# Kernel optimization log

Hardware: AMD Instinct MI355X
Metric: run time of the kernel (lower is better)

The kernel has to match this reference:

```python
import jax, jax.numpy as jnp
import numpy as np

EPS = 1e-6

def _rmsnorm(x, w):
    var = jnp.mean(x * x, axis=-1, keepdims=True)
    return x * jax.lax.rsqrt(var + EPS) * w

def _act_quant(x):
    # per-token int8 absmax quantization (BitNet b1.58)
    scale = 127.0 / jnp.clip(jnp.max(jnp.abs(x), axis=-1, keepdims=True), 1e-5)
    return jnp.round(jnp.clip(x * scale, -128.0, 127.0)) / scale

def _weight_quant(w):
    # per-tensor ternary quantization with mean-abs scale
    scale = 1.0 / jnp.clip(jnp.mean(jnp.abs(w)), 1e-5)
    return jnp.round(jnp.clip(w * scale, -1.0, 1.0)) / scale

def _ste(x, qfn):
    return x + jax.lax.stop_gradient(qfn(x) - x)

def _bitlinear(x, w):
    xq = _ste(x, _act_quant)
    wq = _ste(w, _weight_quant)
    return jnp.einsum('bsh,fh->bsf', xq, wq)

def setup_inputs() -> dict:
    key = jax.random.key(0)
    k1, k2, k3 = jax.random.split(key, 3)
    B, S, H, F = 4, 4096, 1024, 4096
    x = jax.random.normal(k1, (B, S, H), dtype=jnp.float32)
    norm_w = jnp.ones((H,), dtype=jnp.float32)
    w_up = jax.random.normal(k2, (F, H), dtype=jnp.float32) * (H ** -0.5)
    w_down = jax.random.normal(k3, (H, F), dtype=jnp.float32) * (F ** -0.5)
    return {"x": x, "norm_w": norm_w, "w_up": w_up, "w_down": w_down}

def reference(x, norm_w, w_up, w_down):
    residual = x
    h = _rmsnorm(x, norm_w)
    h = _bitlinear(h, w_up)          # [B,S,F]
    h = jnp.square(jax.nn.relu(h))   # relu^2
    h = _bitlinear(h, w_down)        # [B,S,H]
    return h + residual
```

## Files before the change

kernel.cpp:

```cpp
#include <hip/hip_runtime.h>
#include <hip/hip_fp16.h>

#define M_TOK 16384
#define H_DIM 1024
#define F_DIM 4096

typedef __attribute__((ext_vector_type(4))) int int4v;

static const size_t OFF_H2    = 0;
static const size_t OFF_Q2    = OFF_H2   + 134217728ULL;
static const size_t OFF_XQ    = OFF_Q2   + 67108864ULL;
static const size_t OFF_WQU   = OFF_XQ   + 16777216ULL;
static const size_t OFF_WQD   = OFF_WQU  + 4194304ULL;
static const size_t OFF_DQX   = OFF_WQD  + 4194304ULL;
static const size_t OFF_S2    = OFF_DQX  + 65536ULL;
static const size_t OFF_DQ2   = OFF_S2   + 65536ULL;
static const size_t OFF_PMAX  = OFF_DQ2  + 65536ULL;
static const size_t OFF_WPART = OFF_PMAX + 4194304ULL;
static const size_t OFF_WSC   = OFF_WPART+ 8192ULL;
static const size_t WS_NEEDED = OFF_WSC  + 16ULL;

__device__ __forceinline__ void ldg_lds16(const void* g, void* l) {
  __builtin_amdgcn_global_load_lds(
      (const __attribute__((address_space(1))) void*)g,
      (__attribute__((address_space(3))) void*)l, 16, 0, 0);
}

__global__ __launch_bounds__(256) void k_wabs(const float* __restrict__ wu,
                                              const float* __restrict__ wd,
                                              float* __restrict__ part) {
  const int b = blockIdx.x;
  const float* w = (b < 1024) ? wu : wd;
  const int cb = b & 1023;
  const size_t base = (size_t)cb * 4096 + threadIdx.x * 4;
  float s = 0.0f;
#pragma unroll
  for (int it = 0; it < 4; ++it) {
    const float4 v = *(const float4*)(w + base + it * 1024);
    s += fabsf(v.x) + fabsf(v.y) + fabsf(v.z) + fabsf(v.w);
  }
#pragma unroll
  for (int sh = 32; sh; sh >>= 1) s += __shfl_xor(s, sh, 64);
  __shared__ float red[4];
  if ((threadIdx.x & 63) == 0) red[threadIdx.x >> 6] = s;
  __syncthreads();
  if (threadIdx.x == 0) part[b] = red[0] + red[1] + red[2] + red[3];
}

__global__ __launch_bounds__(256) void k_wscale(const float* __restrict__ part,
                                                float* __restrict__ wsc) {
  const int b = blockIdx.x;
  const float* p = part + b * 1024;
  float s = p[threadIdx.x] + p[threadIdx.x + 256] + p[threadIdx.x + 512] + p[threadIdx.x + 768];
#pragma unroll
  for (int sh = 32; sh; sh >>= 1) s += __shfl_xor(s, sh, 64);
  __shared__ float red[4];
  if ((threadIdx.x & 63) == 0) red[threadIdx.x >> 6] = s;
  __syncthreads();
  if (threadIdx.x == 0) {
    const float mean = (red[0] + red[1] + red[2] + red[3]) * (1.0f / 4194304.0f);
    const float c = fmaxf(mean, 1e-5f);
    wsc[b * 2]     = c;
    wsc[b * 2 + 1] = 1.0f / c;
  }
}

__global__ __launch_bounds__(256) void k_wquant(const float* __restrict__ wu,
                                                const float* __restrict__ wd,
                                                char* __restrict__ qu,
                                                char* __restrict__ qd,
                                                const float* __restrict__ wsc) {
  const size_t t = (size_t)blockIdx.x * 256 + threadIdx.x;
  const float* w; char* q; float scale; size_t i;
  if (t < 1048576) { w = wu; q = qu; scale = wsc[1]; i = t * 4; }
  else             { w = wd; q = qd; scale = wsc[3]; i = (t - 1048576) * 4; }
  const float4 v = *(const float4*)(w + i);
  const int a = (int)rintf(fminf(fmaxf(v.x * scale, -1.0f), 1.0f));
  const int b = (int)rintf(fminf(fmaxf(v.y * scale, -1.0f), 1.0f));
  const int c = (int)rintf(fminf(fmaxf(v.z * scale, -1.0f), 1.0f));
  const int d = (int)rintf(fminf(fmaxf(v.w * scale, -1.0f), 1.0f));
  *(unsigned*)(q + i) = (a & 255) | ((b & 255) << 8) | ((c & 255) << 16) | ((d & 255) << 24);
}

__global__ __launch_bounds__(256) void k_rmsnorm_quant(const float* __restrict__ x,
                                                       const float* __restrict__ nw,
                                                       char* __restrict__ xq,
                                                       float* __restrict__ dqx) {
  const int row = blockIdx.x;
  const int t = threadIdx.x;
  const float4 v = *(const float4*)(x + (size_t)row * H_DIM + t * 4);
  float ss = v.x * v.x + v.y * v.y + v.z * v.z + v.w * v.w;
#pragma unroll
  for (int sh = 32; sh; sh >>= 1) ss += __shfl_xor(ss, sh, 64);
  __shared__ float red[4];
  __shared__ float redm[4];
  if ((t & 63) == 0) red[t >> 6] = ss;
  __syncthreads();
  ss = red[0] + red[1] + red[2] + red[3];
  const float rinv = 1.0f / sqrtf(ss * (1.0f / 1024.0f) + 1e-6f);
  const float4 w4 = *(const float4*)(nw + t * 4);
  float4 n;
  n.x = v.x * rinv * w4.x;  n.y = v.y * rinv * w4.y;
  n.z = v.z * rinv * w4.z;  n.w = v.w * rinv * w4.w;
  float am = fmaxf(fmaxf(fabsf(n.x), fabsf(n.y)), fmaxf(fabsf(n.z), fabsf(n.w)));
#pragma unroll
  for (int sh = 32; sh; sh >>= 1) am = fmaxf(am, __shfl_xor(am, sh, 64));
  if ((t & 63) == 0) redm[t >> 6] = am;
  __syncthreads();
  am = fmaxf(fmaxf(redm[0], redm[1]), fmaxf(redm[2], redm[3]));
  am = fmaxf(am, 1e-5f);
  const float scale = 127.0f / am;
  const int qa = (int)rintf(fminf(fmaxf(n.x * scale, -128.0f), 127.0f));
  const int qb = (int)rintf(fminf(fmaxf(n.y * scale, -128.0f), 127.0f));
  const int qc = (int)rintf(fminf(fmaxf(n.z * scale, -128.0f), 127.0f));
  const int qd = (int)rintf(fminf(fmaxf(n.w * scale, -128.0f), 127.0f));
  *(unsigned*)(xq + (size_t)row * H_DIM + t * 4) =
      (qa & 255) | ((qb & 255) << 8) | ((qc & 255) << 16) | ((qd & 255) << 24);
  if (t == 0) dqx[row] = am * (1.0f / 127.0f);
}

template <int LDA_, int LDB_, int KTILES>
__device__ __forceinline__ void gemm_core(const char* __restrict__ A,
                                          const char* __restrict__ B,
                                          int mBase, int nBase,
                                          char* As, char* Bs, int4v acc[4][4]) {
  const int t = threadIdx.x;
  const int lane = t & 63;
  const int wm = (t >> 6) & 1;
  const int wn = t >> 7;
  const int sRow = t >> 2;
  const int sCol = (t & 3) << 4;
  const char* Ag0 = A + (size_t)(mBase + sRow) * LDA_ + sCol;
  const char* Ag1 = A + (size_t)(mBase + 64 + sRow) * LDA_ + sCol;
  const char* Bg0 = B + (size_t)(nBase + sRow) * LDB_ + sCol;
  const char* Bg1 = B + (size_t)(nBase + 64 + sRow) * LDB_ + sCol;
  char* Al0 = As + t * 16;
  char* Al1 = As + 4096 + t * 16;
  char* Bl0 = Bs + t * 16;
  char* Bl1 = Bs + 4096 + t * 16;
  const int aOff = (wm * 64 + (lane & 15)) * 64 + ((lane >> 4) << 4);
  const int bOff = (wn * 64 + (lane & 15)) * 64 + ((lane >> 4) << 4);

  for (int kt = 0; kt < KTILES; ++kt) {
    __syncthreads();
    ldg_lds16(Ag0, Al0);
    ldg_lds16(Ag1, Al1);
    ldg_lds16(Bg0, Bl0);
    ldg_lds16(Bg1, Bl1);
    Ag0 += 64; Ag1 += 64; Bg0 += 64; Bg1 += 64;
    __syncthreads();
    int4v a[4], b[4];
#pragma unroll
    for (int i = 0; i < 4; ++i) a[i] = *(const int4v*)(As + aOff + i * 16 * 64);
#pragma unroll
    for (int j = 0; j < 4; ++j) b[j] = *(const int4v*)(Bs + bOff + j * 16 * 64);
#pragma unroll
    for (int i = 0; i < 4; ++i)
#pragma unroll
      for (int j = 0; j < 4; ++j)
        acc[i][j] = __builtin_amdgcn_mfma_i32_16x16x64_i8(a[i], b[j], acc[i][j], 0, 0, 0);
  }
}

__global__ __launch_bounds__(256, 2) void k_gemm1(const char* __restrict__ xq,
                                                  const char* __restrict__ wq,
                                                  const float* __restrict__ wsc,
                                                  const float* __restrict__ dqx,
                                                  __half* __restrict__ h2,
                                                  float* __restrict__ pmax) {
  __shared__ char smem[16384];
  int4v acc[4][4];
#pragma unroll
  for (int i = 0; i < 4; ++i)
#pragma unroll
    for (int j = 0; j < 4; ++j) acc[i][j] = (int4v){0, 0, 0, 0};
  const int mBase = blockIdx.y * 128;
  const int nBase = blockIdx.x * 128;
  gemm_core<H_DIM, H_DIM, 16>(xq, wq, mBase, nBase, smem, smem + 8192, acc);

  const int t = threadIdx.x;
  const int lane = t & 63;
  const int wm = (t >> 6) & 1;
  const int wn = t >> 7;
  const float dqw = wsc[0];
#pragma unroll
  for (int i = 0; i < 4; ++i) {
    const int rbase = mBase + wm * 64 + i * 16 + ((lane >> 4) << 2);
    const float4 dq4 = *(const float4*)(dqx + rbase);
    const float* dqp = (const float*)&dq4;
    float rmax[4] = {0.0f, 0.0f, 0.0f, 0.0f};
#pragma unroll
    for (int j = 0; j < 4; ++j) {
      const int col = nBase + wn * 64 + j * 16 + (lane & 15);
#pragma unroll
      for (int r = 0; r < 4; ++r) {
        float v = (float)acc[i][j][r] * dqp[r] * dqw;
        v = fmaxf(v, 0.0f);
        v = v * v;
        const __half h = __float2half(v);
        h2[(size_t)(rbase + r) * F_DIM + col] = h;
        rmax[r] = fmaxf(rmax[r], __half2float(h));
      }
    }
#pragma unroll
    for (int s = 1; s < 16; s <<= 1) {
#pragma unroll
      for (int r = 0; r < 4; ++r) rmax[r] = fmaxf(rmax[r], __shfl_xor(rmax[r], s, 64));
    }
    if ((lane & 15) == 0) {
      const int nb2 = blockIdx.x * 2 + wn;
#pragma unroll
      for (int r = 0; r < 4; ++r) pmax[(size_t)nb2 * M_TOK + rbase + r] = rmax[r];
    }
  }
}

__global__ __launch_bounds__(256) void k_rowred(const float* __restrict__ pmax,
                                                float* __restrict__ scale2,
                                                float* __restrict__ dq2) {
  const int row = blockIdx.x * 256 + threadIdx.x;
  float m = 0.0f;
#pragma unroll
  for (int i = 0; i < 64; ++i) m = fmaxf(m, pmax[(size_t)i * M_TOK + row]);
  m = fmaxf(m, 1e-5f);
  scale2[row] = 127.0f / m;
  dq2[row] = m * (1.0f / 127.0f);
}

__global__ __launch_bounds__(256) void k_quant2(const __half* __restrict__ h2,
                                                const float* __restrict__ scale2,
                                                char* __restrict__ q2) {
  const size_t t = (size_t)blockIdx.x * 256 + threadIdx.x;
  const size_t i = t * 8;
  const int row = (int)(i >> 12);
  const float s = scale2[row];
  __half2 hh[4];
  *(float4*)hh = *(const float4*)(h2 + i);
  int q[8];
#pragma unroll
  for (int k = 0; k < 4; ++k) {
    const float lo = __low2float(hh[k]);
    const float hi = __high2float(hh[k]);
    q[2 * k]     = (int)rintf(fminf(lo * s, 127.0f));
    q[2 * k + 1] = (int)rintf(fminf(hi * s, 127.0f));
  }
  const unsigned u0 = (q[0] & 255) | ((q[1] & 255) << 8) | ((q[2] & 255) << 16) | ((q[3] & 255) << 24);
  const unsigned u1 = (q[4] & 255) | ((q[5] & 255) << 8) | ((q[6] & 255) << 16) | ((q[7] & 255) << 24);
  *(uint2*)(q2 + i) = make_uint2(u0, u1);
}

__global__ __launch_bounds__(256, 2) void k_gemm2(const char* __restrict__ q2,
                                                  const char* __restrict__ wq,
                                                  const float* __restrict__ wsc,
                                                  const float* __restrict__ dq2,
                                                  const float* __restrict__ x,
                                                  float* __restrict__ out) {
  __shared__ char smem[16384];
  int4v acc[4][4];
#pragma unroll
  for (int i = 0; i < 4; ++i)
#pragma unroll
    for (int j = 0; j < 4; ++j) acc[i][j] = (int4v){0, 0, 0, 0};
  const int mBase = blockIdx.y * 128;
  const int nBase = blockIdx.x * 128;
  gemm_core<F_DIM, F_DIM, 64>(q2, wq, mBase, nBase, smem, smem + 8192, acc);

  const int t = threadIdx.x;
  const int lane = t & 63;
  const int wm = (t >> 6) & 1;
  const int wn = t >> 7;
  const float dqw = wsc[2];
#pragma unroll
  for (int i = 0; i < 4; ++i) {
    const int rbase = mBase + wm * 64 + i * 16 + ((lane >> 4) << 2);
    const float4 dq4 = *(const float4*)(dq2 + rbase);
    const float* dqp = (const float*)&dq4;
#pragma unroll
    for (int j = 0; j < 4; ++j) {
      const int col = nBase + wn * 64 + j * 16 + (lane & 15);
#pragma unroll
      for (int r = 0; r < 4; ++r) {
        const size_t idx = (size_t)(rbase + r) * H_DIM + col;
        out[idx] = (float)acc[i][j][r] * dqp[r] * dqw + x[idx];
      }
    }
  }
}

extern "C" void kernel_launch(void* const* d_in, const int* in_sizes, int n_in,
                              void* d_out, int out_size, void* d_ws, size_t ws_size,
                              hipStream_t stream) {
  const float* x  = (const float*)d_in[0];
  const float* nw = (const float*)d_in[1];
  const float* wu = (const float*)d_in[2];
  const float* wd = (const float*)d_in[3];
  float* out = (float*)d_out;
  char* ws = (char*)d_ws;
  if (ws_size < WS_NEEDED) return;

  __half* h2     = (__half*)(ws + OFF_H2);
  char* q2       = ws + OFF_Q2;
  char* xq       = ws + OFF_XQ;
  char* wqu      = ws + OFF_WQU;
  char* wqd      = ws + OFF_WQD;
  float* dqx     = (float*)(ws + OFF_DQX);
  float* scale2  = (float*)(ws + OFF_S2);
  float* dq2     = (float*)(ws + OFF_DQ2);
  float* pmax    = (float*)(ws + OFF_PMAX);
  float* wpart   = (float*)(ws + OFF_WPART);
  float* wsc     = (float*)(ws + OFF_WSC);

  k_wabs<<<2048, 256, 0, stream>>>(wu, wd, wpart);
  k_wscale<<<2, 256, 0, stream>>>(wpart, wsc);
  k_wquant<<<8192, 256, 0, stream>>>(wu, wd, wqu, wqd, wsc);
  k_rmsnorm_quant<<<M_TOK, 256, 0, stream>>>(x, nw, xq, dqx);
  k_gemm1<<<dim3(F_DIM / 128, M_TOK / 128), 256, 0, stream>>>(xq, wqu, wsc, dqx, h2, pmax);
  k_rowred<<<M_TOK / 256, 256, 0, stream>>>(pmax, scale2, dq2);
  k_quant2<<<(M_TOK * (F_DIM / 8)) / 256, 256, 0, stream>>>(h2, scale2, q2);
  k_gemm2<<<dim3(H_DIM / 128, M_TOK / 128), 256, 0, stream>>>(q2, wqd, wsc, dq2, x, out);
}
```

Measured before the change: 387.2 us.

## Fuse activation requantization into second GEMM and widen K tiles with swizzled LDS

Removes the separate k_quant2 pass. The second GEMM now reads fp16 relu² activations directly and quantizes them to int8 while staging into LDS, using a half2 FMA magic-number trick (adding 1536) plus a byte perm. Both GEMMs move to 128-byte K tiles with XOR-swizzled LDS rows, register prefetch of the A tile, and an occupancy hint of 3 blocks. This drops a full write and read of the 64MB int8 intermediate. In exchange, each gemm2 block re-reads fp16 A data, which is twice the bytes of int8, for every N tile, and the rounding now happens in half precision, which could differ slightly from the fp32 rintf path.

Measured after the change: 542.6 us. 40.1% more time.

```diff
diff --git a/kernel.cpp b/kernel.cpp
--- a/kernel.cpp
+++ b/kernel.cpp
@@ -8,13 +8,12 @@
 typedef __attribute__((ext_vector_type(4))) int int4v;
 
 static const size_t OFF_H2    = 0;
-static const size_t OFF_Q2    = OFF_H2   + 134217728ULL;
-static const size_t OFF_XQ    = OFF_Q2   + 67108864ULL;
+static const size_t OFF_S2    = OFF_H2   + 134217728ULL;
+static const size_t OFF_XQ    = OFF_S2   + 67108864ULL;
 static const size_t OFF_WQU   = OFF_XQ   + 16777216ULL;
 static const size_t OFF_WQD   = OFF_WQU  + 4194304ULL;
 static const size_t OFF_DQX   = OFF_WQD  + 4194304ULL;
-static const size_t OFF_S2    = OFF_DQX  + 65536ULL;
-static const size_t OFF_DQ2   = OFF_S2   + 65536ULL;
+static const size_t OFF_DQ2   = OFF_DQX  + 65536ULL;
 static const size_t OFF_PMAX  = OFF_DQ2  + 65536ULL;
 static const size_t OFF_WPART = OFF_PMAX + 4194304ULL;
 static const size_t OFF_WSC   = OFF_WPART+ 8192ULL;
@@ -24,6 +23,15 @@
   __builtin_amdgcn_global_load_lds(
       (const __attribute__((address_space(1))) void*)g,
       (__attribute__((address_space(3))) void*)l, 16, 0, 0);
+}
+
+__device__ __forceinline__ unsigned pack_q(unsigned u0, unsigned u1,
+                                           __half2 s2, __half2 c1536) {
+  __half2 h0 = __hfma2(*(const __half2*)&u0, s2, c1536);
+  __half2 h1 = __hfma2(*(const __half2*)&u1, s2, c1536);
+  const unsigned d0 = (*(const unsigned*)&h0) - 0x66006600u;
+  const unsigned d1 = (*(const unsigned*)&h1) - 0x66006600u;
+  return __builtin_amdgcn_perm(d1, d0, 0x06040200u);
 }
 
 __global__ __launch_bounds__(256) void k_wabs(const float* __restrict__ wu,
@@ -119,69 +127,77 @@
   if (t == 0) dqx[row] = am * (1.0f / 127.0f);
 }
 
-template <int LDA_, int LDB_, int KTILES>
-__device__ __forceinline__ void gemm_core(const char* __restrict__ A,
-                                          const char* __restrict__ B,
-                                          int mBase, int nBase,
-                                          char* As, char* Bs, int4v acc[4][4]) {
-  const int t = threadIdx.x;
-  const int lane = t & 63;
-  const int wm = (t >> 6) & 1;
-  const int wn = t >> 7;
-  const int sRow = t >> 2;
-  const int sCol = (t & 3) << 4;
-  const char* Ag0 = A + (size_t)(mBase + sRow) * LDA_ + sCol;
-  const char* Ag1 = A + (size_t)(mBase + 64 + sRow) * LDA_ + sCol;
-  const char* Bg0 = B + (size_t)(nBase + sRow) * LDB_ + sCol;
-  const char* Bg1 = B + (size_t)(nBase + 64 + sRow) * LDB_ + sCol;
-  char* Al0 = As + t * 16;
-  char* Al1 = As + 4096 + t * 16;
-  char* Bl0 = Bs + t * 16;
-  char* Bl1 = Bs + 4096 + t * 16;
-  const int aOff = (wm * 64 + (lane & 15)) * 64 + ((lane >> 4) << 4);
-  const int bOff = (wn * 64 + (lane & 15)) * 64 + ((lane >> 4) << 4);
-
-  for (int kt = 0; kt < KTILES; ++kt) {
-    __syncthreads();
-    ldg_lds16(Ag0, Al0);
-    ldg_lds16(Ag1, Al1);
-    ldg_lds16(Bg0, Bl0);
-    ldg_lds16(Bg1, Bl1);
-    Ag0 += 64; Ag1 += 64; Bg0 += 64; Bg1 += 64;
-    __syncthreads();
-    int4v a[4], b[4];
-#pragma unroll
-    for (int i = 0; i < 4; ++i) a[i] = *(const int4v*)(As + aOff + i * 16 * 64);
-#pragma unroll
-    for (int j = 0; j < 4; ++j) b[j] = *(const int4v*)(Bs + bOff + j * 16 * 64);
-#pragma unroll
-    for (int i = 0; i < 4; ++i)
-#pragma unroll
-      for (int j = 0; j < 4; ++j)
-        acc[i][j] = __builtin_amdgcn_mfma_i32_16x16x64_i8(a[i], b[j], acc[i][j], 0, 0, 0);
-  }
-}
-
-__global__ __launch_bounds__(256, 2) void k_gemm1(const char* __restrict__ xq,
+__global__ __launch_bounds__(256, 3) void k_gemm1(const char* __restrict__ xq,
                                                   const char* __restrict__ wq,
                                                   const float* __restrict__ wsc,
                                                   const float* __restrict__ dqx,
                                                   __half* __restrict__ h2,
                                                   float* __restrict__ pmax) {
-  __shared__ char smem[16384];
+  __shared__ __align__(16) char smem[32768];
+  char* As = smem;
+  char* Bs = smem + 16384;
   int4v acc[4][4];
 #pragma unroll
   for (int i = 0; i < 4; ++i)
 #pragma unroll
     for (int j = 0; j < 4; ++j) acc[i][j] = (int4v){0, 0, 0, 0};
-  const int mBase = blockIdx.y * 128;
-  const int nBase = blockIdx.x * 128;
-  gemm_core<H_DIM, H_DIM, 16>(xq, wq, mBase, nBase, smem, smem + 8192, acc);
-
   const int t = threadIdx.x;
   const int lane = t & 63;
   const int wm = (t >> 6) & 1;
   const int wn = t >> 7;
+  const int nBase = blockIdx.x * 128;
+  const int mBase = blockIdx.y * 128;
+
+  const int aRow = t >> 1;
+  const int aSegBase = (t & 1) * 4;
+  const char* Ag = xq + (size_t)(mBase + aRow) * H_DIM + aSegBase * 16;
+  char* AlBase = As + aRow * 128;
+  uint4 areg[4];
+#pragma unroll
+  for (int n = 0; n < 4; ++n) areg[n] = *(const uint4*)(Ag + n * 16);
+
+  const int bRow = t >> 3;
+  const int bSeg = (t & 7) ^ (bRow & 7);
+  const char* Bg = wq + (size_t)(nBase + bRow) * H_DIM + bSeg * 16;
+  char* Bl = Bs + t * 16;
+
+  const int q = lane >> 4;
+  const int rA = wm * 64 + (lane & 15);
+  const int rB = wn * 64 + (lane & 15);
+  const int swA = rA & 7;
+  const int swB = rB & 7;
+
+  for (int kt = 0; kt < 8; ++kt) {
+    __syncthreads();
+#pragma unroll
+    for (int n = 0; n < 4; ++n) {
+      const int s = aSegBase + n;
+      *(uint4*)(AlBase + ((s ^ (aRow & 7)) << 4)) = areg[n];
+    }
+#pragma unroll
+    for (int n = 0; n < 4; ++n) ldg_lds16(Bg + (size_t)n * 32 * H_DIM, Bl + n * 4096);
+    Bg += 128;
+    __syncthreads();
+    const char* An = Ag + (size_t)(((kt + 1) & 7) * 128);
+#pragma unroll
+    for (int n = 0; n < 4; ++n) areg[n] = *(const uint4*)(An + n * 16);
+#pragma unroll
+    for (int ks = 0; ks < 2; ++ks) {
+      const int ao = (((ks * 4 + q) ^ swA) << 4);
+      const int bo = (((ks * 4 + q) ^ swB) << 4);
+      int4v a[4], b[4];
+#pragma unroll
+      for (int i = 0; i < 4; ++i) a[i] = *(const int4v*)(As + (rA + i * 16) * 128 + ao);
+#pragma unroll
+      for (int j = 0; j < 4; ++j) b[j] = *(const int4v*)(Bs + (rB + j * 16) * 128 + bo);
+#pragma unroll
+      for (int i = 0; i < 4; ++i)
+#pragma unroll
+        for (int j = 0; j < 4; ++j)
+          acc[i][j] = __builtin_amdgcn_mfma_i32_16x16x64_i8(a[i], b[j], acc[i][j], 0, 0, 0);
+    }
+  }
+
   const float dqw = wsc[0];
 #pragma unroll
   for (int i = 0; i < 4; ++i) {
@@ -227,48 +243,87 @@
   dq2[row] = m * (1.0f / 127.0f);
 }
 
-__global__ __launch_bounds__(256) void k_quant2(const __half* __restrict__ h2,
-                                                const float* __restrict__ scale2,
-                                                char* __restrict__ q2) {
-  const size_t t = (size_t)blockIdx.x * 256 + threadIdx.x;
-  const size_t i = t * 8;
-  const int row = (int)(i >> 12);
-  const float s = scale2[row];
-  __half2 hh[4];
-  *(float4*)hh = *(const float4*)(h2 + i);
-  int q[8];
-#pragma unroll
-  for (int k = 0; k < 4; ++k) {
-    const float lo = __low2float(hh[k]);
-    const float hi = __high2float(hh[k]);
-    q[2 * k]     = (int)rintf(fminf(lo * s, 127.0f));
-    q[2 * k + 1] = (int)rintf(fminf(hi * s, 127.0f));
-  }
-  const unsigned u0 = (q[0] & 255) | ((q[1] & 255) << 8) | ((q[2] & 255) << 16) | ((q[3] & 255) << 24);
-  const unsigned u1 = (q[4] & 255) | ((q[5] & 255) << 8) | ((q[6] & 255) << 16) | ((q[7] & 255) << 24);
-  *(uint2*)(q2 + i) = make_uint2(u0, u1);
-}
-
-__global__ __launch_bounds__(256, 2) void k_gemm2(const char* __restrict__ q2,
+__global__ __launch_bounds__(256, 3) void k_gemm2(const __half* __restrict__ h2,
                                                   const char* __restrict__ wq,
                                                   const float* __restrict__ wsc,
                                                   const float* __restrict__ dq2,
+                                                  const float* __restrict__ scale2,
                                                   const float* __restrict__ x,
                                                   float* __restrict__ out) {
-  __shared__ char smem[16384];
+  __shared__ __align__(16) char smem[32768];
+  char* As = smem;
+  char* Bs = smem + 16384;
   int4v acc[4][4];
 #pragma unroll
   for (int i = 0; i < 4; ++i)
 #pragma unroll
     for (int j = 0; j < 4; ++j) acc[i][j] = (int4v){0, 0, 0, 0};
-  const int mBase = blockIdx.y * 128;
-  const int nBase = blockIdx.x * 128;
-  gemm_core<F_DIM, F_DIM, 64>(q2, wq, mBase, nBase, smem, smem + 8192, acc);
-
   const int t = threadIdx.x;
   const int lane = t & 63;
   const int wm = (t >> 6) & 1;
   const int wn = t >> 7;
+  const int nBase = blockIdx.x * 128;
+  const int mBase = blockIdx.y * 128;
+
+  const int aRow = t >> 1;
+  const int aHalf = t & 1;
+  const int aSegBase = aHalf * 4;
+  const __half* Ag = h2 + (size_t)(mBase + aRow) * F_DIM + aHalf * 64;
+  const __half sh = __float2half(scale2[mBase + aRow]);
+  const __half2 s2 = __halves2half2(sh, sh);
+  const __half2 c1536 = __float2half2_rn(1536.0f);
+  char* AlBase = As + aRow * 128;
+  uint4 areg[8];
+#pragma unroll
+  for (int n = 0; n < 8; ++n) areg[n] = *(const uint4*)(Ag + n * 8);
+
+  const int bRow = t >> 3;
+  const int bSeg = (t & 7) ^ (bRow & 7);
+  const char* Bg = wq + (size_t)(nBase + bRow) * F_DIM + bSeg * 16;
+  char* Bl = Bs + t * 16;
+
+  const int q = lane >> 4;
+  const int rA = wm * 64 + (lane & 15);
+  const int rB = wn * 64 + (lane & 15);
+  const int swA = rA & 7;
+  const int swB = rB & 7;
+
+  for (int kt = 0; kt < 32; ++kt) {
+    __syncthreads();
+#pragma unroll
+    for (int m = 0; m < 4; ++m) {
+      uint4 qd;
+      qd.x = pack_q(areg[2 * m].x, areg[2 * m].y, s2, c1536);
+      qd.y = pack_q(areg[2 * m].z, areg[2 * m].w, s2, c1536);
+      qd.z = pack_q(areg[2 * m + 1].x, areg[2 * m + 1].y, s2, c1536);
+      qd.w = pack_q(areg[2 * m + 1].z, areg[2 * m + 1].w, s2, c1536);
+      const int s = aSegBase + m;
+      *(uint4*)(AlBase + ((s ^ (aRow & 7)) << 4)) = qd;
+    }
+#pragma unroll
+    for (int n = 0; n < 4; ++n) ldg_lds16(Bg + (size_t)n * 32 * F_DIM, Bl + n * 4096);
+    Bg += 128;
+    __syncthreads();
+    const __half* An = Ag + (size_t)(((kt + 1) & 31) * 128);
+#pragma unroll
+    for (int n = 0; n < 8; ++n) areg[n] = *(const uint4*)(An + n * 8);
+#pragma unroll
+    for (int ks = 0; ks < 2; ++ks) {
+      const int ao = (((ks * 4 + q) ^ swA) << 4);
+      const int bo = (((ks * 4 + q) ^ swB) << 4);
+      int4v a[4], b[4];
+#pragma unroll
+      for (int i = 0; i < 4; ++i) a[i] = *(const int4v*)(As + (rA + i * 16) * 128 + ao);
+#pragma unroll
+      for (int j = 0; j < 4; ++j) b[j] = *(const int4v*)(Bs + (rB + j * 16) * 128 + bo);
+#pragma unroll
+      for (int i = 0; i < 4; ++i)
+#pragma unroll
+        for (int j = 0; j < 4; ++j)
+          acc[i][j] = __builtin_amdgcn_mfma_i32_16x16x64_i8(a[i], b[j], acc[i][j], 0, 0, 0);
+    }
+  }
+
   const float dqw = wsc[2];
 #pragma unroll
   for (int i = 0; i < 4; ++i) {
@@ -299,12 +354,11 @@
   if (ws_size < WS_NEEDED) return;
 
   __half* h2     = (__half*)(ws + OFF_H2);
-  char* q2       = ws + OFF_Q2;
+  float* scale2  = (float*)(ws + OFF_S2);
   char* xq       = ws + OFF_XQ;
   char* wqu      = ws + OFF_WQU;
   char* wqd      = ws + OFF_WQD;
   float* dqx     = (float*)(ws + OFF_DQX);
-  float* scale2  = (float*)(ws + OFF_S2);
   float* dq2     = (float*)(ws + OFF_DQ2);
   float* pmax    = (float*)(ws + OFF_PMAX);
   float* wpart   = (float*)(ws + OFF_WPART);
@@ -316,6 +370,5 @@
   k_rmsnorm_quant<<<M_TOK, 256, 0, stream>>>(x, nw, xq, dqx);
   k_gemm1<<<dim3(F_DIM / 128, M_TOK / 128), 256, 0, stream>>>(xq, wqu, wsc, dqx, h2, pmax);
   k_rowred<<<M_TOK / 256, 256, 0, stream>>>(pmax, scale2, dq2);
-  k_quant2<<<(M_TOK * (F_DIM / 8)) / 256, 256, 0, stream>>>(h2, scale2, q2);
-  k_gemm2<<<dim3(H_DIM / 128, M_TOK / 128), 256, 0, stream>>>(q2, wqd, wsc, dq2, x, out);
-}
+  k_gemm2<<<dim3(H_DIM / 128, M_TOK / 128), 256, 0, stream>>>(h2, wqd, wsc, dq2, scale2, x, out);
+}
```
